# Performance work log

Measured on AMD Instinct MI355X. Metric: run time of the kernel, lower is better.

Reference implementation:

```python
import jax, jax.numpy as jnp
import numpy as np

N_NODES = 50000
N_EDGES = 800000
N_FEAT = 128
HIDDEN = 64
N_LAYERS = 3
N_GRAPHS = 512
N_CLASSES = 10
BN_EPS = 1e-5


def setup_inputs() -> dict:
    key = jax.random.key(0)
    ks = jax.random.split(key, 16)
    s = 1.0 / np.sqrt(HIDDEN)
    inp = {
        "x": jax.random.normal(ks[0], (N_NODES, N_FEAT), dtype=jnp.float32),
        "edge_index": jax.random.randint(ks[1], (2, N_EDGES), 0, N_NODES, dtype=jnp.int32),
        "batch": jnp.sort(jax.random.randint(ks[2], (N_NODES,), 0, N_GRAPHS, dtype=jnp.int32)),
        "enc_w": jax.random.normal(ks[3], (N_FEAT, HIDDEN), dtype=jnp.float32) / np.sqrt(N_FEAT),
        "enc_b": jnp.zeros((HIDDEN,), dtype=jnp.float32),
        "eps": jnp.zeros((N_LAYERS,), dtype=jnp.float32),
        "conv_w1": jax.random.normal(ks[4], (N_LAYERS, HIDDEN, HIDDEN), dtype=jnp.float32) * s,
        "conv_b1": jnp.zeros((N_LAYERS, HIDDEN), dtype=jnp.float32),
        "conv_w2": jax.random.normal(ks[5], (N_LAYERS, HIDDEN, HIDDEN), dtype=jnp.float32) * s,
        "conv_b2": jnp.zeros((N_LAYERS, HIDDEN), dtype=jnp.float32),
        "bn_gamma": jnp.ones((N_LAYERS, HIDDEN), dtype=jnp.float32),
        "bn_beta": jnp.zeros((N_LAYERS, HIDDEN), dtype=jnp.float32),
        "lin_w": jax.random.normal(ks[6], (HIDDEN, N_CLASSES), dtype=jnp.float32) * s,
        "lin_b": jnp.zeros((N_CLASSES,), dtype=jnp.float32),
    }
    return inp


def reference(x, edge_index, batch, enc_w, enc_b, eps, conv_w1, conv_b1,
              conv_w2, conv_b2, bn_gamma, bn_beta, lin_w, lin_b):
    n = x.shape[0]
    src, dst = edge_index[0], edge_index[1]
    h = x @ enc_w + enc_b  # [N, H] encoder
    for l in range(N_LAYERS):
        # GINConv: sum-aggregate neighbor features, add (1+eps)*self, 2-layer MLP
        agg = jax.ops.segment_sum(h[src], dst, num_segments=n)
        z = (1.0 + eps[l]) * h + agg
        z = jnp.maximum(z @ conv_w1[l] + conv_b1[l], 0.0) @ conv_w2[l] + conv_b2[l]
        # BatchNorm1d (batch statistics) + ReLU; dropout omitted (eval mode)
        mean = jnp.mean(z, axis=0)
        var = jnp.mean(jnp.square(z - mean), axis=0)
        z = (z - mean) * jax.lax.rsqrt(var + BN_EPS) * bn_gamma[l] + bn_beta[l]
        h = jnp.maximum(z, 0.0)
    # global mean pool over graphs
    pooled = jax.ops.segment_sum(h, batch, num_segments=N_GRAPHS)
    counts = jax.ops.segment_sum(jnp.ones((n,), dtype=h.dtype), batch, num_segments=N_GRAPHS)
    pooled = pooled / jnp.maximum(counts, 1.0)[:, None]
    return pooled @ lin_w + lin_b  # [N_GRAPHS, N_CLASSES]
```

## Files before the change

kernel.cpp:

```cpp
#include <hip/hip_runtime.h>

#define N_NODES   50000
#define N_EDGES   800000
#define N_FEAT    128
#define HIDDEN    64
#define N_LAYERS  3
#define N_GRAPHS  512
#define N_CLASSES 10
#define BN_EPS    1e-5f
#define SCAN_BLK  196
#define LWAVES    8
#define HP        32
#define NBLK      782
#define NGRP      (N_NODES / 4)
#define QSCALE    65536.0f
#define QINV      (1.0f / 65536.0f)
#define SSCALE    1048576.0
#define SINV      (1.0 / 1048576.0)

__device__ __forceinline__ int swz(int c, int g) { return g ^ (c & 15); }

__device__ __forceinline__ unsigned bf16rne(float x)
{
    unsigned u = __float_as_uint(x);
    return (u + 0x7fffu + ((u >> 16) & 1u)) >> 16;
}
__device__ __forceinline__ float2 bf2(unsigned u)
{
    float2 r;
    r.x = __uint_as_float(u << 16);
    r.y = __uint_as_float(u & 0xffff0000u);
    return r;
}

__device__ __forceinline__ void accrow(int (&a)[8], uint4 u)
{
    float2 f0 = bf2(u.x), f1 = bf2(u.y), f2 = bf2(u.z), f3 = bf2(u.w);
    a[0] += (int)(f0.x * QSCALE); a[1] += (int)(f0.y * QSCALE);
    a[2] += (int)(f1.x * QSCALE); a[3] += (int)(f1.y * QSCALE);
    a[4] += (int)(f2.x * QSCALE); a[5] += (int)(f2.y * QSCALE);
    a[6] += (int)(f3.x * QSCALE); a[7] += (int)(f3.y * QSCALE);
}

__device__ __forceinline__ void bn_const(const unsigned long long* stats,
                                         const float* gamma, const float* beta,
                                         int c, float& A, float& B)
{
    double m  = (double)(long long)stats[c]          * (SINV / (double)N_NODES);
    double e2 = (double)(long long)stats[HIDDEN + c] * (SINV / (double)N_NODES);
    float mean = (float)m;
    float var  = (float)(e2 - m * m);
    float inv  = rsqrtf(fmaxf(var, 0.f) + BN_EPS);
    A = inv * gamma[c];
    B = beta[c] - mean * A;
}

__global__ __launch_bounds__(512, 6) void enc_kernel(
    const float* __restrict__ x, const float* __restrict__ w,
    const float* __restrict__ b, unsigned* __restrict__ h,
    int* __restrict__ deg)
{
    __shared__ __align__(16) float wT[HIDDEN * N_FEAT];
    __shared__ __align__(16) float xb[LWAVES][4][N_FEAT];
    {
        int g = blockIdx.x * 512 + threadIdx.x;
        if (g < N_NODES) deg[g] = 0;
    }
    for (int i = threadIdx.x; i < N_FEAT * HIDDEN; i += 512) {
        int k = i >> 6, c = i & 63;
        wT[c * 128 + swz(c, k >> 2) * 4 + (k & 3)] = w[i];
    }
    const int lane = threadIdx.x & 63;
    const int wv   = threadIdx.x >> 6;
    const int sz   = lane & 15;
    const int r2   = lane >> 5;
    const int cc   = (lane & 31) * 4;
    const float bias = b[lane];
    __syncthreads();
    const int nwaves = gridDim.x * LWAVES;
    for (int grp = blockIdx.x * LWAVES + wv; grp < NGRP; grp += nwaves) {
        const int nbase = grp * 4;
        float4 v0 = *(const float4*)&x[(size_t)(nbase + r2) * N_FEAT + cc];
        float4 v1 = *(const float4*)&x[(size_t)(nbase + 2 + r2) * N_FEAT + cc];
        *((float4*)&xb[wv][r2][cc])     = v0;
        *((float4*)&xb[wv][2 + r2][cc]) = v1;
        float o0 = bias, o1 = bias, o2 = bias, o3 = bias;
        #pragma unroll 8
        for (int kc = 0; kc < N_FEAT / 4; ++kc) {
            float4 w4 = *(const float4*)&wT[lane * 128 + ((kc ^ sz) << 2)];
            float4 z0 = *(const float4*)&xb[wv][0][4 * kc];
            float4 z1 = *(const float4*)&xb[wv][1][4 * kc];
            float4 z2 = *(const float4*)&xb[wv][2][4 * kc];
            float4 z3 = *(const float4*)&xb[wv][3][4 * kc];
            o0 = fmaf(w4.x, z0.x, fmaf(w4.y, z0.y, fmaf(w4.z, z0.z, fmaf(w4.w, z0.w, o0))));
            o1 = fmaf(w4.x, z1.x, fmaf(w4.y, z1.y, fmaf(w4.z, z1.z, fmaf(w4.w, z1.w, o1))));
            o2 = fmaf(w4.x, z2.x, fmaf(w4.y, z2.y, fmaf(w4.z, z2.z, fmaf(w4.w, z2.w, o2))));
            o3 = fmaf(w4.x, z3.x, fmaf(w4.y, z3.y, fmaf(w4.z, z3.z, fmaf(w4.w, z3.w, o3))));
        }
        float t0 = __shfl_xor(o0, 1), t1 = __shfl_xor(o1, 1);
        float t2 = __shfl_xor(o2, 1), t3 = __shfl_xor(o3, 1);
        if (!(lane & 1)) {
            int p = lane >> 1;
            h[(size_t)(nbase + 0) * HP + p] = bf16rne(o0) | (bf16rne(t0) << 16);
            h[(size_t)(nbase + 1) * HP + p] = bf16rne(o1) | (bf16rne(t1) << 16);
            h[(size_t)(nbase + 2) * HP + p] = bf16rne(o2) | (bf16rne(t2) << 16);
            h[(size_t)(nbase + 3) * HP + p] = bf16rne(o3) | (bf16rne(t3) << 16);
        }
    }
}

__global__ __launch_bounds__(256) void hist_kernel(const int* __restrict__ ei,
                                                   int* __restrict__ deg,
                                                   unsigned long long* __restrict__ stats)
{
    if (blockIdx.x == 0) {
        for (int i = threadIdx.x; i < N_LAYERS * 2 * HIDDEN; i += 256) stats[i] = 0ull;
    }
    int e = blockIdx.x * 256 + threadIdx.x;
    if (e < N_EDGES) atomicAdd(&deg[ei[N_EDGES + e]], 1);
}

__global__ __launch_bounds__(256) void scan1_kernel(const int* __restrict__ deg,
                                                    int* __restrict__ row_start,
                                                    int* __restrict__ bsum)
{
    __shared__ int s[256];
    const int tid = threadIdx.x;
    const int gid = blockIdx.x * 256 + tid;
    int v = (gid < N_NODES) ? deg[gid] : 0;
    s[tid] = v;
    __syncthreads();
    for (int off = 1; off < 256; off <<= 1) {
        int t = (tid >= off) ? s[tid - off] : 0;
        __syncthreads();
        if (tid >= off) s[tid] += t;
        __syncthreads();
    }
    if (gid < N_NODES) row_start[gid] = s[tid] - v;
    if (tid == 255) bsum[blockIdx.x] = s[255];
}

__global__ __launch_bounds__(256) void scan2_kernel(int* __restrict__ bsum,
                                                    int* __restrict__ row_start)
{
    __shared__ int s[256];
    const int tid = threadIdx.x;
    int v = (tid < SCAN_BLK) ? bsum[tid] : 0;
    s[tid] = v;
    __syncthreads();
    for (int off = 1; off < 256; off <<= 1) {
        int t = (tid >= off) ? s[tid - off] : 0;
        __syncthreads();
        if (tid >= off) s[tid] += t;
        __syncthreads();
    }
    if (tid < SCAN_BLK) bsum[tid] = s[tid] - v;
    if (tid == 255) row_start[N_NODES] = s[255];
}

__global__ __launch_bounds__(256) void scan3_kernel(int* __restrict__ row_start,
                                                    const int* __restrict__ bsum,
                                                    int* __restrict__ cursor)
{
    int gid = blockIdx.x * 256 + threadIdx.x;
    if (gid < N_NODES) {
        int v = row_start[gid] + bsum[blockIdx.x];
        row_start[gid] = v;
        cursor[gid] = v;
    }
}

__global__ __launch_bounds__(256) void fill_kernel(const int* __restrict__ ei,
                                                   int* __restrict__ cursor,
                                                   int* __restrict__ csr_src)
{
    int e = blockIdx.x * 256 + threadIdx.x;
    if (e >= N_EDGES) return;
    int d = ei[N_EDGES + e];
    int pos = atomicAdd(&cursor[d], 1);
    csr_src[pos] = ei[e];
}

__global__ __launch_bounds__(512, 8) void layer_kernel(
    const unsigned* __restrict__ hin, const int* __restrict__ csr_src,
    const int* __restrict__ row_start,
    const float* __restrict__ eps, int layer,
    const float* __restrict__ w1, const float* __restrict__ b1,
    const float* __restrict__ w2, const float* __restrict__ b2,
    unsigned* __restrict__ hout, unsigned long long* __restrict__ stats_cur)
{
    __shared__ __align__(16) float wT1[HIDDEN * HIDDEN];
    __shared__ __align__(16) float wT2[HIDDEN * HIDDEN];
    __shared__ __align__(16) float zb[LWAVES][4][HIDDEN];
    for (int i = threadIdx.x; i < HIDDEN * HIDDEN; i += 512) {
        int k = i >> 6, c = i & 63;
        int dst = c * 64 + swz(c, k >> 2) * 4 + (k & 3);
        wT1[dst] = w1[i];
        wT2[dst] = w2[i];
    }
    const int lane = threadIdx.x & 63;
    const int wv   = threadIdx.x >> 6;
    const int o    = lane >> 3;
    const int c8   = (lane & 7) * 4;
    const int cb   = c8 * 2;
    const int sz   = lane & 15;
    const float sf  = 1.0f + eps[layer];
    const float b1c = b1[lane], b2c = b2[lane];
    __syncthreads();

    long long sAcc = 0, s2Acc = 0;
    const int nwaves = gridDim.x * LWAVES;
    for (int grp = blockIdx.x * LWAVES + wv; grp < NGRP; grp += nwaves) {
        const int nbase = grp * 4;
        const int rsv = row_start[nbase + (lane < 5 ? lane : 0)];
        #pragma unroll
        for (int n = 0; n < 4; ++n) {
            const int node = nbase + n;
            const int s0 = __shfl(rsv, n);
            const int s1 = __shfl(rsv, n + 1);
            const uint4 su = *(const uint4*)&hin[(size_t)node * HP + c8];
            int a[8];
            #pragma unroll
            for (int t = 0; t < 8; ++t) a[t] = 0;
            for (int jb = s0; jb < s1; jb += 64) {
                int m = s1 - jb; if (m > 64) m = 64;
                int idx = csr_src[jb + (lane < m ? lane : m - 1)];
                int mm = m & ~7;
                int j = 0;
                for (; j + 16 <= mm; j += 16) {
                    int i0 = __shfl(idx, j + o);
                    int i1 = __shfl(idx, j + 8 + o);
                    uint4 u0 = *(const uint4*)&hin[(size_t)i0 * HP + c8];
                    uint4 u1 = *(const uint4*)&hin[(size_t)i1 * HP + c8];
                    accrow(a, u0);
                    accrow(a, u1);
                }
                for (; j < mm; j += 8) {
                    int i = __shfl(idx, j + o);
                    uint4 u = *(const uint4*)&hin[(size_t)i * HP + c8];
                    accrow(a, u);
                }
                int r8 = m & 7;
                if (r8) {
                    int sl = mm + o;
                    int i = __shfl(idx, sl < m ? sl : m - 1);
                    if (o < r8) {
                        uint4 u = *(const uint4*)&hin[(size_t)i * HP + c8];
                        accrow(a, u);
                    }
                }
            }
            #pragma unroll
            for (int t = 0; t < 8; ++t) {
                a[t] += __shfl_xor(a[t], 8);
                a[t] += __shfl_xor(a[t], 16);
                a[t] += __shfl_xor(a[t], 32);
            }
            if (o == 0) {
                float2 g0 = bf2(su.x), g1 = bf2(su.y), g2 = bf2(su.z), g3 = bf2(su.w);
                float zo[8];
                zo[0] = fmaf(sf, g0.x, (float)a[0] * QINV);
                zo[1] = fmaf(sf, g0.y, (float)a[1] * QINV);
                zo[2] = fmaf(sf, g1.x, (float)a[2] * QINV);
                zo[3] = fmaf(sf, g1.y, (float)a[3] * QINV);
                zo[4] = fmaf(sf, g2.x, (float)a[4] * QINV);
                zo[5] = fmaf(sf, g2.y, (float)a[5] * QINV);
                zo[6] = fmaf(sf, g3.x, (float)a[6] * QINV);
                zo[7] = fmaf(sf, g3.y, (float)a[7] * QINV);
                float4 q0 = {zo[0], zo[1], zo[2], zo[3]};
                float4 q1 = {zo[4], zo[5], zo[6], zo[7]};
                *((float4*)&zb[wv][n][cb])     = q0;
                *((float4*)&zb[wv][n][cb + 4]) = q1;
            }
        }
        float o0 = b1c, o1 = b1c, o2 = b1c, o3 = b1c;
        #pragma unroll 4
        for (int kc = 0; kc < HIDDEN / 4; ++kc) {
            float4 w4 = *(const float4*)&wT1[lane * 64 + ((kc ^ sz) << 2)];
            float4 z0 = *(const float4*)&zb[wv][0][4 * kc];
            float4 z1 = *(const float4*)&zb[wv][1][4 * kc];
            float4 z2 = *(const float4*)&zb[wv][2][4 * kc];
            float4 z3 = *(const float4*)&zb[wv][3][4 * kc];
            o0 = fmaf(w4.x, z0.x, fmaf(w4.y, z0.y, fmaf(w4.z, z0.z, fmaf(w4.w, z0.w, o0))));
            o1 = fmaf(w4.x, z1.x, fmaf(w4.y, z1.y, fmaf(w4.z, z1.z, fmaf(w4.w, z1.w, o1))));
            o2 = fmaf(w4.x, z2.x, fmaf(w4.y, z2.y, fmaf(w4.z, z2.z, fmaf(w4.w, z2.w, o2))));
            o3 = fmaf(w4.x, z3.x, fmaf(w4.y, z3.y, fmaf(w4.z, z3.z, fmaf(w4.w, z3.w, o3))));
        }
        zb[wv][0][lane] = fmaxf(o0, 0.f);
        zb[wv][1][lane] = fmaxf(o1, 0.f);
        zb[wv][2][lane] = fmaxf(o2, 0.f);
        zb[wv][3][lane] = fmaxf(o3, 0.f);
        float p0 = b2c, p1 = b2c, p2 = b2c, p3 = b2c;
        #pragma unroll 4
        for (int kc = 0; kc < HIDDEN / 4; ++kc) {
            float4 w4 = *(const float4*)&wT2[lane * 64 + ((kc ^ sz) << 2)];
            float4 z0 = *(const float4*)&zb[wv][0][4 * kc];
            float4 z1 = *(const float4*)&zb[wv][1][4 * kc];
            float4 z2 = *(const float4*)&zb[wv][2][4 * kc];
            float4 z3 = *(const float4*)&zb[wv][3][4 * kc];
            p0 = fmaf(w4.x, z0.x, fmaf(w4.y, z0.y, fmaf(w4.z, z0.z, fmaf(w4.w, z0.w, p0))));
            p1 = fmaf(w4.x, z1.x, fmaf(w4.y, z1.y, fmaf(w4.z, z1.z, fmaf(w4.w, z1.w, p1))));
            p2 = fmaf(w4.x, z2.x, fmaf(w4.y, z2.y, fmaf(w4.z, z2.z, fmaf(w4.w, z2.w, p2))));
            p3 = fmaf(w4.x, z3.x, fmaf(w4.y, z3.y, fmaf(w4.z, z3.z, fmaf(w4.w, z3.w, p3))));
        }
        float t0 = __shfl_xor(p0, 1), t1 = __shfl_xor(p1, 1);
        float t2 = __shfl_xor(p2, 1), t3 = __shfl_xor(p3, 1);
        if (!(lane & 1)) {
            int p = lane >> 1;
            hout[(size_t)(nbase + 0) * HP + p] = bf16rne(p0) | (bf16rne(t0) << 16);
            hout[(size_t)(nbase + 1) * HP + p] = bf16rne(p1) | (bf16rne(t1) << 16);
            hout[(size_t)(nbase + 2) * HP + p] = bf16rne(p2) | (bf16rne(t2) << 16);
            hout[(size_t)(nbase + 3) * HP + p] = bf16rne(p3) | (bf16rne(t3) << 16);
        }
        float g1 = (p0 + p1) + (p2 + p3);
        float g2 = (p0 * p0 + p1 * p1) + (p2 * p2 + p3 * p3);
        sAcc  += (long long)((double)g1 * SSCALE);
        s2Acc += (long long)((double)g2 * SSCALE);
    }
    __syncthreads();
    long long* red = (long long*)&zb[0][0][0];
    red[threadIdx.x]       = sAcc;
    red[512 + threadIdx.x] = s2Acc;
    __syncthreads();
    if (wv == 0) {
        long long ts = 0, ts2 = 0;
        #pragma unroll
        for (int wq = 0; wq < LWAVES; ++wq) {
            ts  += red[wq * 64 + lane];
            ts2 += red[512 + wq * 64 + lane];
        }
        atomicAdd((unsigned long long*)&stats_cur[lane],          (unsigned long long)ts);
        atomicAdd((unsigned long long*)&stats_cur[HIDDEN + lane], (unsigned long long)ts2);
    }
}

__global__ __launch_bounds__(512) void bn_apply_kernel(
    unsigned* __restrict__ h, const unsigned long long* __restrict__ stats,
    const float* __restrict__ gamma, const float* __restrict__ beta)
{
    int gid = blockIdx.x * 512 + threadIdx.x;
    if (gid >= N_NODES * 8) return;
    const int cb = (gid & 7) * 8;
    float A[8], B[8];
    #pragma unroll
    for (int t = 0; t < 8; ++t) bn_const(stats, gamma, beta, cb + t, A[t], B[t]);
    uint4 u = *((const uint4*)h + gid);
    float2 f0 = bf2(u.x), f1 = bf2(u.y), f2 = bf2(u.z), f3 = bf2(u.w);
    float v[8] = {f0.x, f0.y, f1.x, f1.y, f2.x, f2.y, f3.x, f3.y};
    unsigned w[4];
    #pragma unroll
    for (int t = 0; t < 4; ++t) {
        float lo = fmaxf(fmaf(v[2 * t],     A[2 * t],     B[2 * t]),     0.f);
        float hi = fmaxf(fmaf(v[2 * t + 1], A[2 * t + 1], B[2 * t + 1]), 0.f);
        w[t] = bf16rne(lo) | (bf16rne(hi) << 16);
    }
    uint4 ov = {w[0], w[1], w[2], w[3]};
    *((uint4*)h + gid) = ov;
}

__device__ __forceinline__ int lbound(const int* __restrict__ a, int n, int v)
{
    int lo = 0, hi = n;
    while (lo < hi) { int m = (lo + hi) >> 1; if (a[m] < v) lo = m + 1; else hi = m; }
    return lo;
}

__global__ __launch_bounds__(256) void pool_out_kernel(
    const unsigned* __restrict__ hpre, const int* __restrict__ batch,
    const unsigned long long* __restrict__ stats, const float* __restrict__ gamma,
    const float* __restrict__ beta, const float* __restrict__ lw,
    const float* __restrict__ lb, float* __restrict__ out)
{
    __shared__ int bounds[2];
    __shared__ float red[256];
    __shared__ float pv[64];
    const int g = blockIdx.x;
    if (threadIdx.x < 2)
        bounds[threadIdx.x] = lbound(batch, N_NODES, g + threadIdx.x);
    __syncthreads();
    const int start = bounds[0], end = bounds[1];
    const int col = threadIdx.x & 63;
    const int row = threadIdx.x >> 6;
    float A, B;
    bn_const(stats, gamma, beta, col, A, B);
    float s = 0.f;
    for (int r = start + row; r < end; r += 4) {
        unsigned u = hpre[(size_t)r * HP + (col >> 1)];
        float v = (col & 1) ? __uint_as_float(u & 0xffff0000u)
                            : __uint_as_float(u << 16);
        s += fmaxf(fmaf(v, A, B), 0.f);
    }
    red[threadIdx.x] = s;
    __syncthreads();
    if (row == 0) {
        float t = red[col] + red[64 + col] + red[128 + col] + red[192 + col];
        pv[col] = t / fmaxf((float)(end - start), 1.0f);
    }
    __syncthreads();
    if (threadIdx.x < N_CLASSES) {
        float acc = lb[threadIdx.x];
        #pragma unroll 16
        for (int j = 0; j < HIDDEN; ++j)
            acc = fmaf(pv[j], lw[j * N_CLASSES + threadIdx.x], acc);
        out[g * N_CLASSES + threadIdx.x] = acc;
    }
}

extern "C" void kernel_launch(void* const* d_in, const int* in_sizes, int n_in,
                              void* d_out, int out_size, void* d_ws, size_t ws_size,
                              hipStream_t stream)
{
    const float* x       = (const float*)d_in[0];
    const int*   ei      = (const int*)d_in[1];
    const int*   batch   = (const int*)d_in[2];
    const float* enc_w   = (const float*)d_in[3];
    const float* enc_b   = (const float*)d_in[4];
    const float* eps     = (const float*)d_in[5];
    const float* conv_w1 = (const float*)d_in[6];
    const float* conv_b1 = (const float*)d_in[7];
    const float* conv_w2 = (const float*)d_in[8];
    const float* conv_b2 = (const float*)d_in[9];
    const float* bn_g    = (const float*)d_in[10];
    const float* bn_b    = (const float*)d_in[11];
    const float* lin_w   = (const float*)d_in[12];
    const float* lin_b   = (const float*)d_in[13];
    float* out = (float*)d_out;

    char* ws = (char*)d_ws;
    const size_t HB = (size_t)N_NODES * HP * sizeof(unsigned);
    size_t off = 0;
    unsigned* P    = (unsigned*)(ws + off); off += HB;
    unsigned* Q    = (unsigned*)(ws + off); off += HB;
    unsigned long long* stats64 = (unsigned long long*)(ws + off);
    off += N_LAYERS * 2 * HIDDEN * sizeof(unsigned long long);
    int* deg       = (int*)(ws + off); off += 50176 * sizeof(int);
    int* row_start = (int*)(ws + off); off += 50176 * sizeof(int);
    int* cursor    = (int*)(ws + off); off += 50176 * sizeof(int);
    int* bsum      = (int*)(ws + off); off += 256 * sizeof(int);
    int* csr_src   = (int*)(ws + off); off += (size_t)N_EDGES * sizeof(int);

    enc_kernel<<<768, 512, 0, stream>>>(x, enc_w, enc_b, P, deg);

    hist_kernel<<<(N_EDGES + 255) / 256, 256, 0, stream>>>(ei, deg, stats64);
    scan1_kernel<<<SCAN_BLK, 256, 0, stream>>>(deg, row_start, bsum);
    scan2_kernel<<<1, 256, 0, stream>>>(bsum, row_start);
    scan3_kernel<<<SCAN_BLK, 256, 0, stream>>>(row_start, bsum, cursor);
    fill_kernel<<<(N_EDGES + 255) / 256, 256, 0, stream>>>(ei, cursor, csr_src);

    const int bn_grid = (N_NODES * 8 + 511) / 512;
    const unsigned* curin = P;
    unsigned* curout = Q;
    for (int l = 0; l < N_LAYERS; ++l) {
        const float* w1 = conv_w1 + (size_t)l * HIDDEN * HIDDEN;
        const float* b1 = conv_b1 + (size_t)l * HIDDEN;
        const float* w2 = conv_w2 + (size_t)l * HIDDEN * HIDDEN;
        const float* b2 = conv_b2 + (size_t)l * HIDDEN;
        layer_kernel<<<NBLK, 512, 0, stream>>>(
            curin, csr_src, row_start, eps, l,
            w1, b1, w2, b2, curout, stats64 + (size_t)l * 2 * HIDDEN);
        if (l < N_LAYERS - 1)
            bn_apply_kernel<<<bn_grid, 512, 0, stream>>>(
                curout, stats64 + (size_t)l * 2 * HIDDEN,
                bn_g + (size_t)l * HIDDEN, bn_b + (size_t)l * HIDDEN);
        const unsigned* t = curout; curout = (unsigned*)curin; curin = t;
    }

    pool_out_kernel<<<N_GRAPHS, 256, 0, stream>>>(
        Q, batch, stats64 + (size_t)(N_LAYERS - 1) * 2 * HIDDEN,
        bn_g + (size_t)(N_LAYERS - 1) * HIDDEN, bn_b + (size_t)(N_LAYERS - 1) * HIDDEN,
        lin_w, lin_b, out);
}
```

Measured before the change: 340.4 us.

## Fuse BatchNorm+ReLU of previous layer into neighbor gather; drop bn_apply kernel

Removes the separate bn_apply pass by applying the previous layer's BatchNorm affine and ReLU on the fly to each gathered neighbor row and the self row inside a templated layer kernel. This saves two full read/write sweeps of the hidden buffer and two launches. The cost is extra FMA/max work per gathered edge, and a change in rounding because the normalized values are no longer re-rounded to bf16. The change also alters the LDS swizzle pattern for the transposed weights and raises the layer grid from 782 to 1024 blocks.

```diff
diff --git a/kernel.cpp b/kernel.cpp
--- a/kernel.cpp
+++ b/kernel.cpp
@@ -11,15 +11,13 @@
 #define SCAN_BLK  196
 #define LWAVES    8
 #define HP        32
-#define NBLK      782
+#define NBLK      1024
 #define NGRP      (N_NODES / 4)
 #define QSCALE    65536.0f
 #define QINV      (1.0f / 65536.0f)
 #define SSCALE    1048576.0
 #define SINV      (1.0 / 1048576.0)
 
-__device__ __forceinline__ int swz(int c, int g) { return g ^ (c & 15); }
-
 __device__ __forceinline__ unsigned bf16rne(float x)
 {
     unsigned u = __float_as_uint(x);
@@ -33,13 +31,18 @@
     return r;
 }
 
-__device__ __forceinline__ void accrow(int (&a)[8], uint4 u)
+template<bool HASBN>
+__device__ __forceinline__ void accrow_bn(int (&a)[8], uint4 u,
+                                          const float (&Ag)[8], const float (&Bg)[8])
 {
     float2 f0 = bf2(u.x), f1 = bf2(u.y), f2 = bf2(u.z), f3 = bf2(u.w);
-    a[0] += (int)(f0.x * QSCALE); a[1] += (int)(f0.y * QSCALE);
-    a[2] += (int)(f1.x * QSCALE); a[3] += (int)(f1.y * QSCALE);
-    a[4] += (int)(f2.x * QSCALE); a[5] += (int)(f2.y * QSCALE);
-    a[6] += (int)(f3.x * QSCALE); a[7] += (int)(f3.y * QSCALE);
+    float v[8] = {f0.x, f0.y, f1.x, f1.y, f2.x, f2.y, f3.x, f3.y};
+    #pragma unroll
+    for (int t = 0; t < 8; ++t) {
+        float f = v[t];
+        if (HASBN) f = fmaxf(fmaf(f, Ag[t], Bg[t]), 0.f);
+        a[t] += (int)(f * QSCALE);
+    }
 }
 
 __device__ __forceinline__ void bn_const(const unsigned long long* stats,
@@ -68,11 +71,12 @@
     }
     for (int i = threadIdx.x; i < N_FEAT * HIDDEN; i += 512) {
         int k = i >> 6, c = i & 63;
-        wT[c * 128 + swz(c, k >> 2) * 4 + (k & 3)] = w[i];
+        int szc = (c & 15) ^ ((c >> 4) << 2);
+        wT[c * 128 + (((k >> 2) ^ szc) << 2) + (k & 3)] = w[i];
     }
     const int lane = threadIdx.x & 63;
     const int wv   = threadIdx.x >> 6;
-    const int sz   = lane & 15;
+    const int sz   = (lane & 15) ^ ((lane >> 4) << 2);
     const int r2   = lane >> 5;
     const int cc   = (lane & 31) * 4;
     const float bias = b[lane];
@@ -181,9 +185,12 @@
     csr_src[pos] = ei[e];
 }
 
+template<bool HASBN>
 __global__ __launch_bounds__(512, 8) void layer_kernel(
     const unsigned* __restrict__ hin, const int* __restrict__ csr_src,
     const int* __restrict__ row_start,
+    const unsigned long long* __restrict__ stats_prev,
+    const float* __restrict__ gamma, const float* __restrict__ beta,
     const float* __restrict__ eps, int layer,
     const float* __restrict__ w1, const float* __restrict__ b1,
     const float* __restrict__ w2, const float* __restrict__ b2,
@@ -194,7 +201,8 @@
     __shared__ __align__(16) float zb[LWAVES][4][HIDDEN];
     for (int i = threadIdx.x; i < HIDDEN * HIDDEN; i += 512) {
         int k = i >> 6, c = i & 63;
-        int dst = c * 64 + swz(c, k >> 2) * 4 + (k & 3);
+        int szc = (c & 15) ^ ((c >> 4) << 2);
+        int dst = c * 64 + (((k >> 2) ^ szc) << 2) + (k & 3);
         wT1[dst] = w1[i];
         wT2[dst] = w2[i];
     }
@@ -203,7 +211,15 @@
     const int o    = lane >> 3;
     const int c8   = (lane & 7) * 4;
     const int cb   = c8 * 2;
-    const int sz   = lane & 15;
+    const int sz   = (lane & 15) ^ ((lane >> 4) << 2);
+    float Ag[8], Bg[8];
+    #pragma unroll
+    for (int t = 0; t < 8; ++t) { Ag[t] = 1.f; Bg[t] = 0.f; }
+    if (HASBN) {
+        #pragma unroll
+        for (int t = 0; t < 8; ++t)
+            bn_const(stats_prev, gamma, beta, cb + t, Ag[t], Bg[t]);
+    }
     const float sf  = 1.0f + eps[layer];
     const float b1c = b1[lane], b2c = b2[lane];
     __syncthreads();
@@ -232,13 +248,13 @@
                     int i1 = __shfl(idx, j + 8 + o);
                     uint4 u0 = *(const uint4*)&hin[(size_t)i0 * HP + c8];
                     uint4 u1 = *(const uint4*)&hin[(size_t)i1 * HP + c8];
-                    accrow(a, u0);
-                    accrow(a, u1);
+                    accrow_bn<HASBN>(a, u0, Ag, Bg);
+                    accrow_bn<HASBN>(a, u1, Ag, Bg);
                 }
                 for (; j < mm; j += 8) {
                     int i = __shfl(idx, j + o);
                     uint4 u = *(const uint4*)&hin[(size_t)i * HP + c8];
-                    accrow(a, u);
+                    accrow_bn<HASBN>(a, u, Ag, Bg);
                 }
                 int r8 = m & 7;
                 if (r8) {
@@ -246,7 +262,7 @@
                     int i = __shfl(idx, sl < m ? sl : m - 1);
                     if (o < r8) {
                         uint4 u = *(const uint4*)&hin[(size_t)i * HP + c8];
-                        accrow(a, u);
+                        accrow_bn<HASBN>(a, u, Ag, Bg);
                     }
                 }
             }
@@ -258,15 +274,14 @@
             }
             if (o == 0) {
                 float2 g0 = bf2(su.x), g1 = bf2(su.y), g2 = bf2(su.z), g3 = bf2(su.w);
+                float svv[8] = {g0.x, g0.y, g1.x, g1.y, g2.x, g2.y, g3.x, g3.y};
                 float zo[8];
-                zo[0] = fmaf(sf, g0.x, (float)a[0] * QINV);
-                zo[1] = fmaf(sf, g0.y, (float)a[1] * QINV);
-                zo[2] = fmaf(sf, g1.x, (float)a[2] * QINV);
-                zo[3] = fmaf(sf, g1.y, (float)a[3] * QINV);
-                zo[4] = fmaf(sf, g2.x, (float)a[4] * QINV);
-                zo[5] = fmaf(sf, g2.y, (float)a[5] * QINV);
-                zo[6] = fmaf(sf, g3.x, (float)a[6] * QINV);
-                zo[7] = fmaf(sf, g3.y, (float)a[7] * QINV);
+                #pragma unroll
+                for (int t = 0; t < 8; ++t) {
+                    float f = svv[t];
+                    if (HASBN) f = fmaxf(fmaf(f, Ag[t], Bg[t]), 0.f);
+                    zo[t] = fmaf(sf, f, (float)a[t] * QINV);
+                }
                 float4 q0 = {zo[0], zo[1], zo[2], zo[3]};
                 float4 q1 = {zo[4], zo[5], zo[6], zo[7]};
                 *((float4*)&zb[wv][n][cb])     = q0;
@@ -334,30 +349,6 @@
     }
 }
 
-__global__ __launch_bounds__(512) void bn_apply_kernel(
-    unsigned* __restrict__ h, const unsigned long long* __restrict__ stats,
-    const float* __restrict__ gamma, const float* __restrict__ beta)
-{
-    int gid = blockIdx.x * 512 + threadIdx.x;
-    if (gid >= N_NODES * 8) return;
-    const int cb = (gid & 7) * 8;
-    float A[8], B[8];
-    #pragma unroll
-    for (int t = 0; t < 8; ++t) bn_const(stats, gamma, beta, cb + t, A[t], B[t]);
-    uint4 u = *((const uint4*)h + gid);
-    float2 f0 = bf2(u.x), f1 = bf2(u.y), f2 = bf2(u.z), f3 = bf2(u.w);
-    float v[8] = {f0.x, f0.y, f1.x, f1.y, f2.x, f2.y, f3.x, f3.y};
-    unsigned w[4];
-    #pragma unroll
-    for (int t = 0; t < 4; ++t) {
-        float lo = fmaxf(fmaf(v[2 * t],     A[2 * t],     B[2 * t]),     0.f);
-        float hi = fmaxf(fmaf(v[2 * t + 1], A[2 * t + 1], B[2 * t + 1]), 0.f);
-        w[t] = bf16rne(lo) | (bf16rne(hi) << 16);
-    }
-    uint4 ov = {w[0], w[1], w[2], w[3]};
-    *((uint4*)h + gid) = ov;
-}
-
 __device__ __forceinline__ int lbound(const int* __restrict__ a, int n, int v)
 {
     int lo = 0, hi = n;
@@ -447,7 +438,6 @@
     scan3_kernel<<<SCAN_BLK, 256, 0, stream>>>(row_start, bsum, cursor);
     fill_kernel<<<(N_EDGES + 255) / 256, 256, 0, stream>>>(ei, cursor, csr_src);
 
-    const int bn_grid = (N_NODES * 8 + 511) / 512;
     const unsigned* curin = P;
     unsigned* curout = Q;
     for (int l = 0; l < N_LAYERS; ++l) {
@@ -455,13 +445,17 @@
         const float* b1 = conv_b1 + (size_t)l * HIDDEN;
         const float* w2 = conv_w2 + (size_t)l * HIDDEN * HIDDEN;
         const float* b2 = conv_b2 + (size_t)l * HIDDEN;
-        layer_kernel<<<NBLK, 512, 0, stream>>>(
-            curin, csr_src, row_start, eps, l,
-            w1, b1, w2, b2, curout, stats64 + (size_t)l * 2 * HIDDEN);
-        if (l < N_LAYERS - 1)
-            bn_apply_kernel<<<bn_grid, 512, 0, stream>>>(
-                curout, stats64 + (size_t)l * 2 * HIDDEN,
-                bn_g + (size_t)l * HIDDEN, bn_b + (size_t)l * HIDDEN);
+        if (l == 0)
+            layer_kernel<false><<<NBLK, 512, 0, stream>>>(
+                curin, csr_src, row_start, nullptr, nullptr, nullptr,
+                eps, l, w1, b1, w2, b2, curout, stats64);
+        else
+            layer_kernel<true><<<NBLK, 512, 0, stream>>>(
+                curin, csr_src, row_start,
+                stats64 + (size_t)(l - 1) * 2 * HIDDEN,
+                bn_g + (size_t)(l - 1) * HIDDEN, bn_b + (size_t)(l - 1) * HIDDEN,
+                eps, l, w1, b1, w2, b2, curout,
+                stats64 + (size_t)l * 2 * HIDDEN);
         const unsigned* t = curout; curout = (unsigned*)curin; curin = t;
     }
 
```

Measured after the change: 397.5 us. 16.8% more time.
